# Performance work log

Hardware: AMD Instinct MI355X
Metric: run time of the kernel (lower is better)

Reference implementation:

```python
import jax, jax.numpy as jnp
import numpy as np

B, SQ, SKV, E, H = 4, 2048, 2048, 1024, 16
HD = E // H  # 64


def stablemax(x):
    # StableMax: s(x) = x+1 if x>=0 else 1/(1-x), normalized along last axis
    s = jnp.where(x >= 0, x + 1.0, 1.0 / (1.0 - x))
    return s / jnp.sum(s, axis=-1, keepdims=True)


def setup_inputs() -> dict:
    key = jax.random.key(0)
    ks = jax.random.split(key, 6)
    scale = 1.0 / np.sqrt(E)
    return {
        "query": jax.random.normal(ks[0], (B, SQ, E), jnp.float32),
        "key_value": jax.random.normal(ks[1], (B, SKV, E), jnp.float32),
        "Wq": jax.random.normal(ks[2], (E, E), jnp.float32) * scale,
        "bq": jnp.zeros((E,), jnp.float32),
        "Wk": jax.random.normal(ks[3], (E, E), jnp.float32) * scale,
        "bk": jnp.zeros((E,), jnp.float32),
        "Wv": jax.random.normal(ks[4], (E, E), jnp.float32) * scale,
        "bv": jnp.zeros((E,), jnp.float32),
        "Wo": jax.random.normal(ks[5], (E, E), jnp.float32) * scale,
        "bo": jnp.zeros((E,), jnp.float32),
    }


def reference(query, key_value, Wq, bq, Wk, bk, Wv, bv, Wo, bo):
    b = query.shape[0]
    # linear projections (torch Linear: x @ W^T + b)
    q = query @ Wq.T + bq
    k = key_value @ Wk.T + bk
    v = key_value @ Wv.T + bv
    # [B, H, S, HD]
    q = q.reshape(b, -1, H, HD).transpose(0, 2, 1, 3)
    k = k.reshape(b, -1, H, HD).transpose(0, 2, 1, 3)
    v = v.reshape(b, -1, H, HD).transpose(0, 2, 1, 3)
    scores = jnp.einsum("bhqd,bhkd->bhqk", q, k) / np.sqrt(HD).astype(np.float32)
    attn = stablemax(scores)  # dropout is identity in eval mode
    context = jnp.einsum("bhqk,bhkd->bhqd", attn, v)
    context = context.transpose(0, 2, 1, 3).reshape(b, -1, E)
    return context @ Wo.T + bo
```

## Files before the change

kernel.cpp:

```cpp
#include <hip/hip_runtime.h>

typedef __bf16 bf16;
typedef __bf16 bf16x8 __attribute__((ext_vector_type(8)));
typedef __bf16 bf16x4 __attribute__((ext_vector_type(4)));
typedef _Float16 f16;
typedef _Float16 f16x2 __attribute__((ext_vector_type(2)));
typedef _Float16 f16x4 __attribute__((ext_vector_type(4)));
typedef _Float16 f16x8 __attribute__((ext_vector_type(8)));
typedef float f32x4 __attribute__((ext_vector_type(4)));

__device__ __forceinline__ f32x4 mfma_qk(bf16x8 a, bf16x8 b, f32x4 c) {
    return __builtin_amdgcn_mfma_f32_16x16x32_bf16(a, b, c, 0, 0, 0);
}
__device__ __forceinline__ f32x4 mfma_pv32(f16x8 a, f16x8 b, f32x4 c) {
    return __builtin_amdgcn_mfma_f32_16x16x32_f16(a, b, c, 0, 0, 0);
}

#define GLOAD_LDS16(gp, lp)                                                    \
    __builtin_amdgcn_global_load_lds(                                          \
        (const __attribute__((address_space(1))) unsigned int*)(gp),           \
        (__attribute__((address_space(3))) unsigned int*)(lp), 16, 0, 0)

__global__ __launch_bounds__(256) void cast_inputs(
    const float* __restrict__ w0, const float* __restrict__ w1,
    const float* __restrict__ w2, const float* __restrict__ w3,
    const float* __restrict__ kv, const float* __restrict__ q,
    bf16* __restrict__ Wb, bf16* __restrict__ KVa, bf16* __restrict__ Qb) {
    long i4 = (long)blockIdx.x * 256 + threadIdx.x;
    const float* src;
    bf16* dst;
    long loc;
    if (i4 < 1048576) {
        int which = (int)(i4 >> 18);
        loc = (i4 & 262143) << 2;
        src = which == 0 ? w0 : which == 1 ? w1 : which == 2 ? w2 : w3;
        dst = Wb + ((long)which << 20);
    } else if (i4 < 3145728) {
        loc = (i4 - 1048576) << 2;
        src = kv; dst = KVa;
    } else {
        loc = (i4 - 3145728) << 2;
        src = q; dst = Qb;
    }
    float4 f = *(const float4*)(src + loc);
    bf16x4 o;
    o[0] = (bf16)f.x; o[1] = (bf16)f.y; o[2] = (bf16)f.z; o[3] = (bf16)f.w;
    *(bf16x4*)(dst + loc) = o;
}

__device__ __forceinline__ void gemm_core(
    const bf16* __restrict__ A, const bf16* __restrict__ Wt,
    const float* __restrict__ bias, void* __restrict__ Yv,
    const int om, bf16* smem, const int n0, const int m0) {
    constexpr int Kd = 1024, Nd = 1024;
    constexpr int TP = 132;
    bf16* As = smem;
    bf16* Bs = smem + 8192;
    const int tid = threadIdx.x;
    const int wid = tid >> 6, lane = tid & 63;
    const int l16 = lane & 15, quad = lane >> 4;
    const int mh = (wid >> 1) * 64, nh = (wid & 1) * 64;

    f32x4 acc[4][4];
#pragma unroll
    for (int i = 0; i < 4; ++i)
#pragma unroll
        for (int j = 0; j < 4; ++j) acc[i][j] = (f32x4){0.f, 0.f, 0.f, 0.f};

    for (int k0 = 0; k0 < Kd; k0 += 64) {
#pragma unroll
        for (int j = 0; j < 4; ++j) {
            const int s = j * 256 + tid;
            const int r = s >> 3, c8 = (s & 7) ^ (r & 7);
            GLOAD_LDS16(A + (long)(m0 + r) * Kd + k0 + c8 * 8, &As[s * 8]);
            GLOAD_LDS16(Wt + (long)(n0 + r) * Kd + k0 + c8 * 8, &Bs[s * 8]);
        }
        __syncthreads();
#pragma unroll
        for (int kc = 0; kc < 2; ++kc) {
            bf16x8 af[4], bq[4];
#pragma unroll
            for (int i = 0; i < 4; ++i) {
                const int row = mh + i * 16 + l16;
                af[i] = *(const bf16x8*)&As[(row * 8 + ((kc * 4 + quad) ^ (row & 7))) * 8];
            }
#pragma unroll
            for (int i = 0; i < 4; ++i) {
                const int row = nh + i * 16 + l16;
                bq[i] = *(const bf16x8*)&Bs[(row * 8 + ((kc * 4 + quad) ^ (row & 7))) * 8];
            }
#pragma unroll
            for (int i = 0; i < 4; ++i)
#pragma unroll
                for (int j = 0; j < 4; ++j)
                    acc[i][j] = mfma_qk(af[i], bq[j], acc[i][j]);
        }
        __syncthreads();
    }

    if (om == 2) {
#pragma unroll
        for (int j = 0; j < 4; ++j) {
            const int col = nh + j * 16 + l16;
            const float bv = bias[n0 + col];
#pragma unroll
            for (int i = 0; i < 4; ++i)
#pragma unroll
                for (int p = 0; p < 2; ++p) {
                    f16x2 pk2;
                    pk2[0] = (f16)(acc[i][j][p * 2 + 0] + bv);
                    pk2[1] = (f16)(acc[i][j][p * 2 + 1] + bv);
                    *(f16x2*)&smem[col * TP + mh + i * 16 + quad * 4 + p * 2] = pk2;
                }
        }
        __syncthreads();
        const int b_ = m0 >> 11, skv0 = m0 & 2047;
        const int rowc = tid & 15;
#pragma unroll
        for (int c = 0; c < 8; ++c) {
            const int col = (tid >> 4) + c * 16;
            const int colg = n0 + col;
            bf16x8 v = *(const bf16x8*)&smem[col * TP + rowc * 8];
            const long base = ((long)((b_ * 16 + (colg >> 6)) * 64 + (colg & 63))) << 11;
            *(bf16x8*)((bf16*)Yv + base + skv0 + rowc * 8) = v;
        }
    } else {
#pragma unroll
        for (int j = 0; j < 4; ++j) {
            const int col = n0 + nh + j * 16 + l16;
            const float bv = bias[col];
#pragma unroll
            for (int i = 0; i < 4; ++i)
#pragma unroll
                for (int r = 0; r < 4; ++r) {
                    int row = m0 + mh + i * 16 + quad * 4 + r;
                    float v = acc[i][j][r] + bv;
                    if (om == 1)
                        ((float*)Yv)[(long)row * Nd + col] = v;
                    else
                        ((bf16*)Yv)[(long)row * Nd + col] = (bf16)v;
                }
        }
    }
}

__global__ __launch_bounds__(256) void proj_qkv(
    const bf16* __restrict__ Qb, const bf16* __restrict__ KVa,
    const bf16* __restrict__ Wb,
    const float* __restrict__ bq, const float* __restrict__ bk,
    const float* __restrict__ bv,
    bf16* __restrict__ Qw, bf16* __restrict__ Kw, f16* __restrict__ Vt) {
    __shared__ __align__(16) bf16 smem[16896];
    const int lin = blockIdx.x + (blockIdx.y << 3) + (blockIdx.z << 9);
    const int nid = (lin & 7) * 192 + (lin >> 3);
    const int z = nid >> 9, rem = nid & 511;
    const int n0 = (rem & 7) << 7, m0 = (rem >> 3) << 7;
    if (z == 0)
        gemm_core(Qb, Wb, bq, Qw, 0, smem, n0, m0);
    else if (z == 1)
        gemm_core(KVa, Wb + (1l << 20), bk, Kw, 0, smem, n0, m0);
    else
        gemm_core(KVa, Wb + (2l << 20), bv, Vt, 2, smem, n0, m0);
}

__global__ __launch_bounds__(256) void gemm_o(
    const bf16* __restrict__ Cw, const bf16* __restrict__ Wo,
    const float* __restrict__ bo, float* __restrict__ out) {
    __shared__ __align__(16) bf16 smem[16896];
    const int lin = blockIdx.x + (blockIdx.y << 3);
    const int nid = (lin & 7) * 64 + (lin >> 3);
    gemm_core(Cw, Wo, bo, out, 1, smem, (nid & 7) << 7, (nid >> 3) << 7);
}

__global__ __launch_bounds__(256) void attn_kernel(
    const bf16* __restrict__ Q, const bf16* __restrict__ K,
    const f16* __restrict__ Vt, bf16* __restrict__ C) {
    constexpr int E = 1024, S = 2048;
    __shared__ __align__(16) char smem_raw[32768];
    bf16* Ks = (bf16*)smem_raw;
    f16* VTs = (f16*)(smem_raw + 16384);

    const int tid = threadIdx.x;
    const int wid = tid >> 6, lane = tid & 63;
    const int l16 = lane & 15, quad = lane >> 4;
    const int lin = blockIdx.x + (blockIdx.y << 4) + (blockIdx.z << 8);
    const int nid = (lin & 7) * 128 + (lin >> 3);
    const int qt = nid & 15, h = (nid >> 4) & 15, b = nid >> 8;

    const long q0 = (long)b * S + qt * 128;
    const bf16* Qg = Q + q0 * E + h * 64;
    const bf16* Kg = K + (long)b * S * E + h * 64;
    const f16* Vg = Vt + ((long)(b * 16 + h) << 17);

    bf16x8 qf[2][2];
#pragma unroll
    for (int mt = 0; mt < 2; ++mt)
#pragma unroll
        for (int kc = 0; kc < 2; ++kc)
            qf[mt][kc] = *(const bf16x8*)(Qg + (long)(wid * 32 + mt * 16 + l16) * E + kc * 32 + quad * 8);

    f32x4 ctx[2][4];
    float den[2] = {0.f, 0.f};
#pragma unroll
    for (int mt = 0; mt < 2; ++mt)
#pragma unroll
        for (int dt = 0; dt < 4; ++dt) ctx[mt][dt] = (f32x4){0.f, 0.f, 0.f, 0.f};

    for (int kv0 = 0; kv0 < S; kv0 += 128) {
#pragma unroll
        for (int j = 0; j < 4; ++j) {
            const int s = j * 256 + tid;
            const int r = s >> 3, c8 = (s & 7) ^ (r & 7);
            GLOAD_LDS16(Kg + (long)(kv0 + r) * E + c8 * 8, &Ks[s * 8]);
        }
#pragma unroll
        for (int j = 0; j < 4; ++j) {
            const int s = j * 256 + tid;
            const int r = s >> 4, c16 = (s & 15) ^ (r & 15);
            GLOAD_LDS16(Vg + (long)r * S + kv0 + c16 * 8, &VTs[s * 8]);
        }
        __syncthreads();

#pragma unroll
        for (int kvp = 0; kvp < 4; ++kvp) {
            f32x4 sacc[2][2];
#pragma unroll
            for (int s = 0; s < 2; ++s) {
                const int rk = kvp * 32 + s * 16 + l16, rb = rk & 7;
                bf16x8 kf0 = *(const bf16x8*)&Ks[(rk * 8 + (quad ^ rb)) * 8];
                bf16x8 kf1 = *(const bf16x8*)&Ks[(rk * 8 + ((quad + 4) ^ rb)) * 8];
                __builtin_amdgcn_s_setprio(1);
#pragma unroll
                for (int mt = 0; mt < 2; ++mt) {
                    f32x4 t = mfma_qk(kf0, qf[mt][0], (f32x4){0.f, 0.f, 0.f, 0.f});
                    sacc[s][mt] = mfma_qk(kf1, qf[mt][1], t);
                }
                __builtin_amdgcn_s_setprio(0);
            }
            f16x8 pp[2];
#pragma unroll
            for (int mt = 0; mt < 2; ++mt) {
#pragma unroll
                for (int s = 0; s < 2; ++s) {
                    float sv[4];
#pragma unroll
                    for (int r = 0; r < 4; ++r) {
                        float x = sacc[s][mt][r];
                        float u = __builtin_fmaf(__builtin_fabsf(x), 0.125f, 1.0f);
                        sv[r] = (x >= 0.f) ? u : __builtin_amdgcn_rcpf(u);
                        pp[mt][s * 4 + r] = (f16)sv[r];
                    }
                    den[mt] += (sv[0] + sv[1]) + (sv[2] + sv[3]);
                }
            }
            const int c16l = 4 * kvp + (quad >> 1), ho = (quad & 1) * 4;
#pragma unroll
            for (int dt = 0; dt < 4; ++dt) {
                const int rv = dt * 16 + l16;
                f16x4 vlo = *(const f16x4*)&VTs[(rv * 16 + (c16l ^ l16)) * 8 + ho];
                f16x4 vhi = *(const f16x4*)&VTs[(rv * 16 + ((c16l + 2) ^ l16)) * 8 + ho];
                f16x8 vf = __builtin_shufflevector(vlo, vhi, 0, 1, 2, 3, 4, 5, 6, 7);
                __builtin_amdgcn_s_setprio(1);
#pragma unroll
                for (int mt = 0; mt < 2; ++mt)
                    ctx[mt][dt] = mfma_pv32(vf, pp[mt], ctx[mt][dt]);
                __builtin_amdgcn_s_setprio(0);
            }
        }
        __syncthreads();
    }

    float scl[2];
#pragma unroll
    for (int mt = 0; mt < 2; ++mt) {
        float d = den[mt];
        d += __shfl_xor(d, 16);
        d += __shfl_xor(d, 32);
        scl[mt] = __builtin_amdgcn_rcpf(d);
    }

    bf16* Os = (bf16*)smem_raw;
#pragma unroll
    for (int mt = 0; mt < 2; ++mt)
#pragma unroll
        for (int dt = 0; dt < 4; ++dt) {
            bf16x4 o;
#pragma unroll
            for (int r = 0; r < 4; ++r) o[r] = (bf16)(ctx[mt][dt][r] * scl[mt]);
            *(bf16x4*)&Os[(wid * 32 + mt * 16 + l16) * 68 + dt * 16 + quad * 4] = o;
        }
    __syncthreads();
    {
        const int r = tid >> 1, c = (tid & 1) * 32;
        bf16* cp = C + (q0 + r) * E + h * 64 + c;
#pragma unroll
        for (int j = 0; j < 4; ++j)
            *(bf16x8*)(cp + j * 8) = *(const bf16x8*)&Os[r * 68 + c + j * 8];
    }
}

extern "C" void kernel_launch(void* const* d_in, const int* in_sizes, int n_in,
                              void* d_out, int out_size, void* d_ws, size_t ws_size,
                              hipStream_t stream) {
    const float* query = (const float*)d_in[0];
    const float* keyv  = (const float*)d_in[1];
    const float* Wq = (const float*)d_in[2];
    const float* bq = (const float*)d_in[3];
    const float* Wk = (const float*)d_in[4];
    const float* bk = (const float*)d_in[5];
    const float* Wv = (const float*)d_in[6];
    const float* bv = (const float*)d_in[7];
    const float* Wo = (const float*)d_in[8];
    const float* bo = (const float*)d_in[9];

    char* ws = (char*)d_ws;
    bf16* Wb  = (bf16*)ws;
    bf16* KVa = (bf16*)(ws + (8l << 20));
    bf16* Qb  = (bf16*)(ws + (24l << 20));
    bf16* Qw  = (bf16*)(ws + (40l << 20));
    f16*  Vt  = (f16*)(ws + (56l << 20));
    bf16* Kw  = (bf16*)d_out;
    bf16* Cw  = KVa;

    cast_inputs<<<20480, 256, 0, stream>>>(Wq, Wk, Wv, Wo, keyv, query, Wb, KVa, Qb);

    proj_qkv<<<dim3(8, 64, 3), 256, 0, stream>>>(Qb, KVa, Wb, bq, bk, bv, Qw, Kw, Vt);

    attn_kernel<<<dim3(16, 16, 4), 256, 0, stream>>>(Qw, Kw, Vt, Cw);

    gemm_o<<<dim3(8, 64), 256, 0, stream>>>(Cw, Wb + (3l << 20), bo, (float*)d_out);
}
```

Measured before the change: 336.8 us.

## Double-buffer K/V tiles in attention and compute denominator via MFMA

The attention loop now uses 64-row KV tiles in two LDS buffers, prefetching the next tile with async global-to-LDS loads while computing the current one, synchronised with explicit waitcnt and barrier. The StableMax denominator is accumulated with an MFMA against a ones vector instead of scalar adds plus a final shuffle reduction. The V-transpose store in the projection GEMM is reordered so each lane reads a contiguous 16-byte f16x8 from LDS during attention. The goals are to hide load latency and cut VALU and LDS instruction count. The risks are the hand-written vmcnt counts and an extra MFMA per step.

```diff
diff --git a/kernel.cpp b/kernel.cpp
--- a/kernel.cpp
+++ b/kernel.cpp
@@ -116,13 +116,17 @@
         __syncthreads();
         const int b_ = m0 >> 11, skv0 = m0 & 2047;
         const int rowc = tid & 15;
+        const int B32 = (rowc >> 2) * 32, g4 = (rowc & 3) * 4;
+        const f16* sm = (const f16*)smem;
 #pragma unroll
         for (int c = 0; c < 8; ++c) {
             const int col = (tid >> 4) + c * 16;
             const int colg = n0 + col;
-            bf16x8 v = *(const bf16x8*)&smem[col * TP + rowc * 8];
+            f16x4 lo = *(const f16x4*)&sm[col * TP + B32 + g4];
+            f16x4 hi = *(const f16x4*)&sm[col * TP + B32 + 16 + g4];
+            f16x8 v = __builtin_shufflevector(lo, hi, 0, 1, 2, 3, 4, 5, 6, 7);
             const long base = ((long)((b_ * 16 + (colg >> 6)) * 64 + (colg & 63))) << 11;
-            *(bf16x8*)((bf16*)Yv + base + skv0 + rowc * 8) = v;
+            *(f16x8*)((f16*)Yv + base + skv0 + rowc * 8) = v;
         }
     } else {
 #pragma unroll
@@ -175,10 +179,12 @@
 __global__ __launch_bounds__(256) void attn_kernel(
     const bf16* __restrict__ Q, const bf16* __restrict__ K,
     const f16* __restrict__ Vt, bf16* __restrict__ C) {
-    constexpr int E = 1024, S = 2048;
+    constexpr int E = 1024, S = 2048, KVB = 64;
     __shared__ __align__(16) char smem_raw[32768];
-    bf16* Ks = (bf16*)smem_raw;
-    f16* VTs = (f16*)(smem_raw + 16384);
+    bf16* Ks0 = (bf16*)smem_raw;
+    bf16* Ks1 = (bf16*)(smem_raw + 8192);
+    f16* Vt0 = (f16*)(smem_raw + 16384);
+    f16* Vt1 = (f16*)(smem_raw + 24576);
 
     const int tid = threadIdx.x;
     const int wid = tid >> 6, lane = tid & 63;
@@ -199,67 +205,72 @@
         for (int kc = 0; kc < 2; ++kc)
             qf[mt][kc] = *(const bf16x8*)(Qg + (long)(wid * 32 + mt * 16 + l16) * E + kc * 32 + quad * 8);
 
+    f16x8 ones8;
+#pragma unroll
+    for (int j = 0; j < 8; ++j) ones8[j] = (f16)1.0f;
+
     f32x4 ctx[2][4];
-    float den[2] = {0.f, 0.f};
-#pragma unroll
-    for (int mt = 0; mt < 2; ++mt)
+    f32x4 dacc[2];
+#pragma unroll
+    for (int mt = 0; mt < 2; ++mt) {
+        dacc[mt] = (f32x4){0.f, 0.f, 0.f, 0.f};
 #pragma unroll
         for (int dt = 0; dt < 4; ++dt) ctx[mt][dt] = (f32x4){0.f, 0.f, 0.f, 0.f};
-
-    for (int kv0 = 0; kv0 < S; kv0 += 128) {
-#pragma unroll
-        for (int j = 0; j < 4; ++j) {
+    }
+
+    auto stage = [&](int kv0, bf16* Kd, f16* Vd) {
+#pragma unroll
+        for (int j = 0; j < 2; ++j) {
             const int s = j * 256 + tid;
             const int r = s >> 3, c8 = (s & 7) ^ (r & 7);
-            GLOAD_LDS16(Kg + (long)(kv0 + r) * E + c8 * 8, &Ks[s * 8]);
-        }
-#pragma unroll
-        for (int j = 0; j < 4; ++j) {
+            GLOAD_LDS16(Kg + (long)(kv0 + r) * E + c8 * 8, &Kd[s * 8]);
+        }
+#pragma unroll
+        for (int j = 0; j < 2; ++j) {
             const int s = j * 256 + tid;
-            const int r = s >> 4, c16 = (s & 15) ^ (r & 15);
-            GLOAD_LDS16(Vg + (long)r * S + kv0 + c16 * 8, &VTs[s * 8]);
-        }
-        __syncthreads();
-
-#pragma unroll
-        for (int kvp = 0; kvp < 4; ++kvp) {
+            const int r = s >> 3, c8 = (s & 7) ^ (r & 7);
+            GLOAD_LDS16(Vg + (long)r * S + kv0 + c8 * 8, &Vd[s * 8]);
+        }
+    };
+
+    auto compute = [&](const bf16* Kc, const f16* Vc) {
+#pragma unroll
+        for (int kvp = 0; kvp < 2; ++kvp) {
             f32x4 sacc[2][2];
 #pragma unroll
-            for (int s = 0; s < 2; ++s) {
-                const int rk = kvp * 32 + s * 16 + l16, rb = rk & 7;
-                bf16x8 kf0 = *(const bf16x8*)&Ks[(rk * 8 + (quad ^ rb)) * 8];
-                bf16x8 kf1 = *(const bf16x8*)&Ks[(rk * 8 + ((quad + 4) ^ rb)) * 8];
+            for (int sh = 0; sh < 2; ++sh) {
+                const int rk = kvp * 32 + sh * 16 + l16, rb = rk & 7;
+                bf16x8 kf0 = *(const bf16x8*)&Kc[(rk * 8 + (quad ^ rb)) * 8];
+                bf16x8 kf1 = *(const bf16x8*)&Kc[(rk * 8 + ((quad + 4) ^ rb)) * 8];
                 __builtin_amdgcn_s_setprio(1);
 #pragma unroll
                 for (int mt = 0; mt < 2; ++mt) {
                     f32x4 t = mfma_qk(kf0, qf[mt][0], (f32x4){0.f, 0.f, 0.f, 0.f});
-                    sacc[s][mt] = mfma_qk(kf1, qf[mt][1], t);
+                    sacc[sh][mt] = mfma_qk(kf1, qf[mt][1], t);
                 }
                 __builtin_amdgcn_s_setprio(0);
             }
             f16x8 pp[2];
 #pragma unroll
-            for (int mt = 0; mt < 2; ++mt) {
-#pragma unroll
-                for (int s = 0; s < 2; ++s) {
-                    float sv[4];
+            for (int mt = 0; mt < 2; ++mt)
+#pragma unroll
+                for (int sh = 0; sh < 2; ++sh)
 #pragma unroll
                     for (int r = 0; r < 4; ++r) {
-                        float x = sacc[s][mt][r];
+                        float x = sacc[sh][mt][r];
                         float u = __builtin_fmaf(__builtin_fabsf(x), 0.125f, 1.0f);
-                        sv[r] = (x >= 0.f) ? u : __builtin_amdgcn_rcpf(u);
-                        pp[mt][s * 4 + r] = (f16)sv[r];
+                        float sv = (x >= 0.f) ? u : __builtin_amdgcn_rcpf(u);
+                        pp[mt][sh * 4 + r] = (f16)sv;
                     }
-                    den[mt] += (sv[0] + sv[1]) + (sv[2] + sv[3]);
-                }
-            }
-            const int c16l = 4 * kvp + (quad >> 1), ho = (quad & 1) * 4;
+            __builtin_amdgcn_s_setprio(1);
+            dacc[0] = mfma_pv32(ones8, pp[0], dacc[0]);
+            dacc[1] = mfma_pv32(ones8, pp[1], dacc[1]);
+            __builtin_amdgcn_s_setprio(0);
+            const int cL = 4 * kvp + quad;
 #pragma unroll
             for (int dt = 0; dt < 4; ++dt) {
                 const int rv = dt * 16 + l16;
-                f16x4 vlo = *(const f16x4*)&VTs[(rv * 16 + (c16l ^ l16)) * 8 + ho];
-                f16x4 vhi = *(const f16x4*)&VTs[(rv * 16 + ((c16l + 2) ^ l16)) * 8 + ho];
-                f16x8 vf = __builtin_shufflevector(vlo, vhi, 0, 1, 2, 3, 4, 5, 6, 7);
+                f16x8 vf = *(const f16x8*)&Vc[(rv * 8 + (cL ^ (rv & 7))) * 8];
                 __builtin_amdgcn_s_setprio(1);
 #pragma unroll
                 for (int mt = 0; mt < 2; ++mt)
@@ -267,17 +278,24 @@
                 __builtin_amdgcn_s_setprio(0);
             }
         }
-        __syncthreads();
-    }
+    };
+
+    stage(0, Ks0, Vt0);
+#pragma unroll 1
+    for (int t = 0; t < 31; ++t) {
+        const int sel = t & 1;
+        stage((t + 1) * KVB, sel ? Ks0 : Ks1, sel ? Vt0 : Vt1);
+        asm volatile("s_waitcnt vmcnt(4)\ns_barrier" ::: "memory");
+        compute(sel ? Ks1 : Ks0, sel ? Vt1 : Vt0);
+        asm volatile("s_waitcnt lgkmcnt(0)\ns_barrier" ::: "memory");
+    }
+    asm volatile("s_waitcnt vmcnt(0)\ns_barrier" ::: "memory");
+    compute(Ks1, Vt1);
+    __syncthreads();
 
     float scl[2];
 #pragma unroll
-    for (int mt = 0; mt < 2; ++mt) {
-        float d = den[mt];
-        d += __shfl_xor(d, 16);
-        d += __shfl_xor(d, 32);
-        scl[mt] = __builtin_amdgcn_rcpf(d);
-    }
+    for (int mt = 0; mt < 2; ++mt) scl[mt] = __builtin_amdgcn_rcpf(dacc[mt][0]);
 
     bf16* Os = (bf16*)smem_raw;
 #pragma unroll
```

After: 329.5 us. 1.02x faster.
